# Optimization experiments

Hardware: AMD Instinct MI355X
Metric: run time of the kernel (lower is better)

Reference implementation:

```python
import jax, jax.numpy as jnp
import numpy as np

D_MODEL = 2048
HEADS = 32
HEAD_DIM = 64   # D_MODEL // HEADS
STATE = 256
KCONV = 4
CHUNK = 64
EPS = 1e-5
CONV_DIM = D_MODEL + 2 * STATE          # 2560 (n_groups=1)
PROJ = D_MODEL + CONV_DIM + HEADS       # 4640 (z | xBC | dt)
BATCH, SEQ = 2, 2048


def rmsnorm(x, w, eps=EPS):
    return x * jax.lax.rsqrt(jnp.mean(x * x, axis=-1, keepdims=True) + eps) * w


def setup_inputs() -> dict:
    key = jax.random.key(0)
    ks = jax.random.split(key, 8)
    x = jax.random.normal(ks[0], (BATCH, SEQ, D_MODEL), jnp.float32)
    norm_w = jnp.ones((D_MODEL,), jnp.float32)
    w_in = jax.random.normal(ks[1], (D_MODEL, PROJ), jnp.float32) * 0.02
    conv_w = jax.random.normal(ks[2], (CONV_DIM, KCONV), jnp.float32) * 0.2
    conv_b = jnp.zeros((CONV_DIM,), jnp.float32)
    # HF-style dt init: softplus(dt_bias) uniform-log in [1e-3, 1e-1]
    dt0 = jnp.exp(jax.random.uniform(ks[3], (HEADS,)) * (np.log(0.1) - np.log(0.001)) + np.log(0.001))
    dt_bias = dt0 + jnp.log(-jnp.expm1(-dt0))
    A_log = jnp.log(jnp.arange(1, HEADS + 1, dtype=jnp.float32))
    D_skip = jnp.ones((HEADS,), jnp.float32)
    gnorm_w = jnp.ones((D_MODEL,), jnp.float32)
    w_out = jax.random.normal(ks[4], (D_MODEL, D_MODEL), jnp.float32) * 0.02
    wo_w = jax.random.normal(ks[5], (D_MODEL, D_MODEL), jnp.float32) * 0.02
    return {"x": x, "norm_w": norm_w, "w_in": w_in, "conv_w": conv_w, "conv_b": conv_b,
            "dt_bias": dt_bias, "A_log": A_log, "D_skip": D_skip, "gnorm_w": gnorm_w,
            "w_out": w_out, "wo_w": wo_w}


def reference(x, norm_w, w_in, conv_w, conv_b, dt_bias, A_log, D_skip, gnorm_w, w_out, wo_w):
    b, L, _ = x.shape
    nc = L // CHUNK
    # pre-RMSNorm
    xn = rmsnorm(x, norm_w)
    # in_proj and split: z | xBC | dt
    proj = xn @ w_in
    z = proj[..., :D_MODEL]
    xBC = proj[..., D_MODEL:D_MODEL + CONV_DIM]
    dt = proj[..., D_MODEL + CONV_DIM:]                      # [b,L,H]
    # causal depthwise conv1d (kernel 4) + SiLU
    xp = jnp.pad(xBC, ((0, 0), (KCONV - 1, 0), (0, 0)))
    conv = conv_b + sum(xp[:, k:k + L] * conv_w[:, k] for k in range(KCONV))
    conv = jax.nn.silu(conv)
    xs = conv[..., :D_MODEL].reshape(b, L, HEADS, HEAD_DIM)  # SSM input
    Bm = conv[..., D_MODEL:D_MODEL + STATE]                  # [b,L,N] (n_groups=1)
    Cm = conv[..., D_MODEL + STATE:]                         # [b,L,N]
    dt = jax.nn.softplus(dt + dt_bias)                       # [b,L,H], >0
    A = -jnp.exp(A_log)                                      # [H]
    # ---- Mamba2 chunked selective scan (chunk_size=64) ----
    def ck(a):
        return a.reshape(b, nc, CHUNK, *a.shape[2:])
    xs_c, dt_c, B_c, C_c = ck(xs), ck(dt), ck(Bm), ck(Cm)
    Adt = dt_c * A                                           # [b,c,l,h] (<=0)
    Acs = jnp.cumsum(Adt, axis=2)
    # intra-chunk (diagonal blocks)
    seg = Acs[:, :, :, None, :] - Acs[:, :, None, :, :]      # [b,c,l,s,h]
    idx = jnp.arange(CHUNK)
    mask = (idx[:, None] >= idx[None, :])[None, None, :, :, None]
    Lmat = jnp.where(mask, jnp.exp(seg), 0.0)                # [b,c,l,s,h]
    CB = jnp.einsum('bcln,bcsn->bcls', C_c, B_c)
    xt = xs_c * dt_c[..., None]                              # [b,c,l,h,p]
    Y_diag = jnp.einsum('bclsh,bcshp->bclhp', CB[..., None] * Lmat, xt)
    # chunk-final states
    decay_states = jnp.exp(Acs[:, :, -1:, :] - Acs)          # [b,c,l,h]
    states = jnp.einsum('bcln,bclh,bclhp->bchpn', B_c, decay_states, xt)
    # inter-chunk recurrence (scan over nc chunks only)
    chunk_decay = jnp.exp(Acs[:, :, -1, :])                  # [b,c,h]
    def step(S, inp):
        dec, st = inp
        return S * dec[:, :, None, None] + st, S
    S0 = jnp.zeros((b, HEADS, HEAD_DIM, STATE), x.dtype)
    _, prev = jax.lax.scan(step, S0, (jnp.moveaxis(chunk_decay, 1, 0), jnp.moveaxis(states, 1, 0)))
    prev = jnp.moveaxis(prev, 0, 1)                          # [b,c,h,p,n] state at chunk start
    Y_off = jnp.einsum('bcln,bchpn,bclh->bclhp', C_c, prev, jnp.exp(Acs))
    y = (Y_diag + Y_off).reshape(b, L, HEADS, HEAD_DIM) + D_skip[None, None, :, None] * xs
    y = y.reshape(b, L, D_MODEL)
    # gated RMSNorm, out_proj, then wo
    y = rmsnorm(y * jax.nn.silu(z), gnorm_w)
    return (y @ w_out) @ wo_w
```

## Files before the change

### kernel.cpp

```cpp
#include <hip/hip_runtime.h>
#include <math.h>

#define D_MODEL 2048
#define HEADS 32
#define HEAD_DIM 64
#define STATE 256
#define KCONV 4
#define CHUNK 64
#define NC 32
#define SEQL 2048
#define BATCHN 2
#define CONV_DIMN 2560
#define PROJ_DIM 4640
#define PROJB_W 4608
#define EPSF 1e-5f
#define BL (BATCHN * SEQL)

typedef __attribute__((ext_vector_type(8))) short short8;
typedef __attribute__((ext_vector_type(4))) short short4v;
typedef __attribute__((ext_vector_type(4))) float f32x4;

__device__ __forceinline__ short f2bf(float f) {
  unsigned u = __builtin_bit_cast(unsigned, f);
  u = (u + 0x7fffu + ((u >> 16) & 1u)) >> 16;
  return (short)u;
}
__device__ __forceinline__ float b2f(short s) {
  unsigned u = ((unsigned)(unsigned short)s) << 16;
  return __builtin_bit_cast(float, u);
}
__device__ __forceinline__ void gld16(const void* g, void* l) {
  __builtin_amdgcn_global_load_lds((const __attribute__((address_space(1))) unsigned int*)g,
                                   (__attribute__((address_space(3))) unsigned int*)l,
                                   16, 0, 0);
}

__global__ __launch_bounds__(256) void rmsnorm_bf16_k(const float* __restrict__ x,
                                                      const float* __restrict__ w,
                                                      short* __restrict__ out) {
  int row = blockIdx.x;
  int t = threadIdx.x;
  const float4* x4 = (const float4*)(x + (size_t)row * D_MODEL);
  float4 va = x4[2 * t], vb = x4[2 * t + 1];
  float ss = va.x * va.x + va.y * va.y + va.z * va.z + va.w * va.w +
             vb.x * vb.x + vb.y * vb.y + vb.z * vb.z + vb.w * vb.w;
  #pragma unroll
  for (int off = 32; off > 0; off >>= 1) ss += __shfl_down(ss, off);
  __shared__ float ws_[4];
  if ((t & 63) == 0) ws_[t >> 6] = ss;
  __syncthreads();
  float tot = ws_[0] + ws_[1] + ws_[2] + ws_[3];
  float scale = rsqrtf(tot / (float)D_MODEL + EPSF);
  const float4* w4 = (const float4*)w;
  float4 wa = w4[2 * t], wb = w4[2 * t + 1];
  short tmp[8];
  tmp[0] = f2bf(va.x * scale * wa.x); tmp[1] = f2bf(va.y * scale * wa.y);
  tmp[2] = f2bf(va.z * scale * wa.z); tmp[3] = f2bf(va.w * scale * wa.w);
  tmp[4] = f2bf(vb.x * scale * wb.x); tmp[5] = f2bf(vb.y * scale * wb.y);
  tmp[6] = f2bf(vb.z * scale * wb.z); tmp[7] = f2bf(vb.w * scale * wb.w);
  *(int4*)(out + (size_t)row * D_MODEL + t * 8) = *(int4*)tmp;
}

__global__ __launch_bounds__(256) void transpose_bf16_k(const float* __restrict__ W,
                                                        short* __restrict__ WT,
                                                        int K, int ncols, int stride) {
  __shared__ float tile[32][33];
  int bn = blockIdx.x * 32, bk = blockIdx.y * 32;
  int tx = threadIdx.x & 31, ty = threadIdx.x >> 5;
  #pragma unroll
  for (int i = 0; i < 32; i += 8) {
    int k = bk + ty + i, n = bn + tx;
    tile[ty + i][tx] = (n < ncols) ? W[(size_t)k * stride + n] : 0.f;
  }
  __syncthreads();
  #pragma unroll
  for (int i = 0; i < 32; i += 8) {
    int n = bn + ty + i, k = bk + tx;
    if (n < ncols) WT[(size_t)n * K + k] = f2bf(tile[tx][ty + i]);
  }
}

__global__ __launch_bounds__(256) void dtg_k(const short* __restrict__ xnb,
                                             const short* __restrict__ wdtT,
                                             float* __restrict__ dtraw) {
  __shared__ float red[4][32][32];
  int t = threadIdx.x;
  int lane = t & 63, w = t >> 6;
  int mr = lane & 15, q = lane >> 4;
  int m0 = blockIdx.x * 32;
  f32x4 acc[2][2] = {};
  for (int ks = 0; ks < 16; ks++) {
    int k = w * 512 + ks * 32 + q * 8;
    short8 af[2], bfr[2];
    #pragma unroll
    for (int i = 0; i < 2; i++)
      af[i] = *(const short8*)&xnb[(size_t)(m0 + i * 16 + mr) * D_MODEL + k];
    #pragma unroll
    for (int i = 0; i < 2; i++)
      bfr[i] = *(const short8*)&wdtT[(size_t)(i * 16 + mr) * D_MODEL + k];
    #pragma unroll
    for (int mi = 0; mi < 2; mi++)
      #pragma unroll
      for (int ni = 0; ni < 2; ni++)
        acc[mi][ni] = __builtin_amdgcn_mfma_f32_16x16x32_bf16(af[mi], bfr[ni], acc[mi][ni], 0, 0, 0);
  }
  #pragma unroll
  for (int mi = 0; mi < 2; mi++)
    #pragma unroll
    for (int ni = 0; ni < 2; ni++)
      #pragma unroll
      for (int r = 0; r < 4; r++)
        red[w][mi * 16 + q * 4 + r][ni * 16 + mr] = acc[mi][ni][r];
  __syncthreads();
  #pragma unroll
  for (int i = 0; i < 4; i++) {
    int e = t + 256 * i;
    int row = e >> 5, col = e & 31;
    dtraw[(size_t)(m0 + row) * HEADS + col] =
        red[0][row][col] + red[1][row][col] + red[2][row][col] + red[3][row][col];
  }
}

template<bool BF16OUT>
__global__ __launch_bounds__(512, 4) void gemm128_k(const short* __restrict__ A,
                                                    const short* __restrict__ BT,
                                                    void* __restrict__ Cout,
                                                    int M, int N, int K) {
  constexpr int ABUF = 128 * 32;
  constexpr int BUFS = ABUF + 8192;
  constexpr int LPT = 3;
  __shared__ short lds[3 * BUFS];

  const int t = threadIdx.x;
  const int lane = t & 63, w = t >> 6;
  const int mr = lane & 15, q = lane >> 4;
  const int cq8 = (q ^ ((mr >> 1) & 3)) * 8;
  const int stj = ((lane & 3) ^ ((lane >> 3) & 3)) * 8;
  const int str = lane >> 2;

  const int nbx = N >> 8;
  const int nwg = nbx * (M >> 7);
  const int cpx = nwg >> 3;
  const int bid = blockIdx.x;
  const int swz = (bid & 7) * cpx + (bid >> 3);
  const int bx = swz % nbx, by = swz / nbx;
  const int m0 = by * 128, n0 = bx * 256;

  const int NT = K >> 5;
  f32x4 acc[8][2] = {};

  auto STAGE = [&](int tile, int buf) {
    short* dst = &lds[buf * BUFS];
    const int kb = tile * 32 + stj;
    gld16(A + (size_t)(m0 + w * 16 + str) * K + kb, dst + w * 512);
    const short* gB = BT + (size_t)(n0 + w * 32 + str) * K + kb;
    short* dB = dst + ABUF + w * 1024;
    gld16(gB, dB);
    gld16(gB + (size_t)16 * K, dB + 512);
  };

  STAGE(0, 0); STAGE(1, 1);
  asm volatile("s_waitcnt vmcnt(%0)" :: "n"(LPT) : "memory");
  __builtin_amdgcn_s_barrier();

  int bufc = 0;
  for (int tt = 0; tt < NT; ++tt) {
    const short* sA = &lds[bufc * BUFS];
    const short* sB = sA + ABUF;
    if (tt + 2 < NT) STAGE(tt + 2, bufc >= 1 ? bufc - 1 : 2);
    short8 af[4], bfr[2];
    #pragma unroll
    for (int ni = 0; ni < 2; ni++)
      bfr[ni] = *(const short8*)&sB[(w * 32 + ni * 16 + mr) * 32 + cq8];
    #pragma unroll
    for (int mi = 0; mi < 4; mi++)
      af[mi] = *(const short8*)&sA[(mi * 16 + mr) * 32 + cq8];
    __builtin_amdgcn_s_setprio(1);
    #pragma unroll
    for (int mi = 0; mi < 4; mi++)
      #pragma unroll
      for (int ni = 0; ni < 2; ni++)
        acc[mi][ni] = __builtin_amdgcn_mfma_f32_16x16x32_bf16(af[mi], bfr[ni], acc[mi][ni], 0, 0, 0);
    __builtin_amdgcn_s_setprio(0);
    #pragma unroll
    for (int mi = 0; mi < 4; mi++)
      af[mi] = *(const short8*)&sA[(64 + mi * 16 + mr) * 32 + cq8];
    __builtin_amdgcn_s_setprio(1);
    #pragma unroll
    for (int mi = 0; mi < 4; mi++)
      #pragma unroll
      for (int ni = 0; ni < 2; ni++)
        acc[4 + mi][ni] = __builtin_amdgcn_mfma_f32_16x16x32_bf16(af[mi], bfr[ni], acc[4 + mi][ni], 0, 0, 0);
    __builtin_amdgcn_s_setprio(0);
    __builtin_amdgcn_sched_barrier(0);
    if (tt + 2 < NT) asm volatile("s_waitcnt vmcnt(%0)" :: "n"(LPT) : "memory");
    else             asm volatile("s_waitcnt vmcnt(0)" ::: "memory");
    __builtin_amdgcn_s_barrier();
    bufc = (bufc == 2) ? 0 : bufc + 1;
  }

  #pragma unroll
  for (int mi = 0; mi < 8; mi++)
    #pragma unroll
    for (int ni = 0; ni < 2; ni++) {
      const int gm = m0 + mi * 16 + q * 4;
      const int gn = n0 + w * 32 + ni * 16 + mr;
      #pragma unroll
      for (int r = 0; r < 4; r++) {
        if (BF16OUT) ((short*)Cout)[(size_t)(gm + r) * N + gn] = f2bf(acc[mi][ni][r]);
        else         ((float*)Cout)[(size_t)(gm + r) * N + gn] = acc[mi][ni][r];
      }
    }
}

template<bool BF16OUT>
__global__ __launch_bounds__(256, 3) void gemm_t128_k(const short* __restrict__ A,
                                                      const short* __restrict__ BT,
                                                      void* __restrict__ Cout,
                                                      int M, int N, int K) {
  constexpr int ABUF = 128 * 32;
  constexpr int BUFS = ABUF + 128 * 32;
  constexpr int LPT = 4;
  __shared__ short lds[3 * BUFS];

  const int t = threadIdx.x;
  const int lane = t & 63, w = t >> 6;
  const int mr = lane & 15, q = lane >> 4;
  const int cq8 = (q ^ ((mr >> 1) & 3)) * 8;
  const int stj = ((lane & 3) ^ ((lane >> 3) & 3)) * 8;
  const int str = lane >> 2;

  const int nbx = N >> 7;
  const int nwg = nbx * (M >> 7);
  const int cpx = nwg >> 3;
  const int bid = blockIdx.x;
  const int swz = (bid & 7) * cpx + (bid >> 3);
  const int bx = swz % nbx, by = swz / nbx;
  const int m0 = by * 128, n0 = bx * 128;

  const int NT = K >> 5;
  f32x4 acc[8][2] = {};

  auto STAGE = [&](int tile, int buf) {
    short* dst = &lds[buf * BUFS];
    const int kb = tile * 32 + stj;
    #pragma unroll
    for (int cc = 0; cc < 2; cc++) {
      gld16(A + (size_t)(m0 + w * 32 + cc * 16 + str) * K + kb,
            dst + (w * 32 + cc * 16) * 32);
      gld16(BT + (size_t)(n0 + w * 32 + cc * 16 + str) * K + kb,
            dst + ABUF + (w * 32 + cc * 16) * 32);
    }
  };

  STAGE(0, 0); STAGE(1, 1);
  asm volatile("s_waitcnt vmcnt(%0)" :: "n"(LPT) : "memory");
  __builtin_amdgcn_s_barrier();

  int bufc = 0;
  for (int tt = 0; tt < NT; ++tt) {
    const short* sA = &lds[bufc * BUFS];
    const short* sB = sA + ABUF;
    if (tt + 2 < NT) STAGE(tt + 2, bufc >= 1 ? bufc - 1 : 2);
    short8 af[4], bfr[2];
    #pragma unroll
    for (int ni = 0; ni < 2; ni++)
      bfr[ni] = *(const short8*)&sB[(w * 32 + ni * 16 + mr) * 32 + cq8];
    #pragma unroll
    for (int mi = 0; mi < 4; mi++)
      af[mi] = *(const short8*)&sA[(mi * 16 + mr) * 32 + cq8];
    __builtin_amdgcn_s_setprio(1);
    #pragma unroll
    for (int mi = 0; mi < 4; mi++)
      #pragma unroll
      for (int ni = 0; ni < 2; ni++)
        acc[mi][ni] = __builtin_amdgcn_mfma_f32_16x16x32_bf16(af[mi], bfr[ni], acc[mi][ni], 0, 0, 0);
    __builtin_amdgcn_s_setprio(0);
    #pragma unroll
    for (int mi = 0; mi < 4; mi++)
      af[mi] = *(const short8*)&sA[(64 + mi * 16 + mr) * 32 + cq8];
    __builtin_amdgcn_s_setprio(1);
    #pragma unroll
    for (int mi = 0; mi < 4; mi++)
      #pragma unroll
      for (int ni = 0; ni < 2; ni++)
        acc[4 + mi][ni] = __builtin_amdgcn_mfma_f32_16x16x32_bf16(af[mi], bfr[ni], acc[4 + mi][ni], 0, 0, 0);
    __builtin_amdgcn_s_setprio(0);
    __builtin_amdgcn_sched_barrier(0);
    if (tt + 2 < NT) asm volatile("s_waitcnt vmcnt(%0)" :: "n"(LPT) : "memory");
    else             asm volatile("s_waitcnt vmcnt(0)" ::: "memory");
    __builtin_amdgcn_s_barrier();
    bufc = (bufc == 2) ? 0 : bufc + 1;
  }

  #pragma unroll
  for (int mi = 0; mi < 8; mi++)
    #pragma unroll
    for (int ni = 0; ni < 2; ni++) {
      const int gm = m0 + mi * 16 + q * 4;
      const int gn = n0 + w * 32 + ni * 16 + mr;
      #pragma unroll
      for (int r = 0; r < 4; r++) {
        if (BF16OUT) ((short*)Cout)[(size_t)(gm + r) * N + gn] = f2bf(acc[mi][ni][r]);
        else         ((float*)Cout)[(size_t)(gm + r) * N + gn] = acc[mi][ni][r];
      }
    }
}

__global__ __launch_bounds__(256) void conv_silu_k(const short* __restrict__ projb,
                                                   const float* __restrict__ cw,
                                                   const float* __restrict__ cb,
                                                   short* __restrict__ out) {
  int idx = blockIdx.x * 256 + threadIdx.x;
  int ci = idx % (CONV_DIMN / 8);
  int bt = idx / (CONV_DIMN / 8);
  int t = bt & (SEQL - 1);
  int b = bt >> 11;
  int c = ci * 8;
  float4 w4[8];
  #pragma unroll
  for (int j = 0; j < 8; j++) w4[j] = ((const float4*)cw)[c + j];
  float acc[8];
  {
    float4 b0 = ((const float4*)(cb + c))[0], b1 = ((const float4*)(cb + c))[1];
    acc[0] = b0.x; acc[1] = b0.y; acc[2] = b0.z; acc[3] = b0.w;
    acc[4] = b1.x; acc[5] = b1.y; acc[6] = b1.z; acc[7] = b1.w;
  }
  #pragma unroll
  for (int k = 0; k < KCONV; k++) {
    int tt = t - (KCONV - 1) + k;
    if (tt < 0) continue;
    short8 v = *(const short8*)&projb[((size_t)(b * SEQL + tt)) * PROJB_W + D_MODEL + c];
    #pragma unroll
    for (int j = 0; j < 8; j++) {
      float wv = (k == 0) ? w4[j].x : (k == 1) ? w4[j].y : (k == 2) ? w4[j].z : w4[j].w;
      acc[j] += b2f(v[j]) * wv;
    }
  }
  short o[8];
  #pragma unroll
  for (int j = 0; j < 8; j++) o[j] = f2bf(acc[j] / (1.f + expf(-acc[j])));
  *(int4*)&out[(size_t)bt * CONV_DIMN + c] = *(int4*)o;
}

__global__ __launch_bounds__(256) void dt_acs_k(const float* __restrict__ dtraw,
                                                const float* __restrict__ dt_bias,
                                                const float* __restrict__ A_log,
                                                float* __restrict__ dtb, float* __restrict__ acsb) {
  int bc = blockIdx.x;
  int b = bc / NC, c = bc % NC;
  int t = threadIdx.x;
  int l = t & 63, w = t >> 6;
  size_t base = ((size_t)(b * SEQL + c * CHUNK + l)) * HEADS;
  #pragma unroll
  for (int i = 0; i < 8; i++) {
    int h = w * 8 + i;
    float raw = dtraw[base + h] + dt_bias[h];
    float dt = raw > 20.f ? raw : log1pf(expf(raw));
    float adt = -expf(A_log[h]) * dt;
    float cs = adt;
    #pragma unroll
    for (int off = 1; off < 64; off <<= 1) {
      float v = __shfl_up(cs, off);
      if (l >= off) cs += v;
    }
    dtb[base + h] = dt;
    acsb[base + h] = cs;
  }
}

__global__ __launch_bounds__(256) void cb_k(const short* __restrict__ convb,
                                            short* __restrict__ CB) {
  int bc = blockIdx.x;
  int b = bc / NC, c = bc % NC;
  __shared__ float sC[64][65];
  __shared__ float sB[64][65];
  int t = threadIdx.x;
  int s = t & 63;
  int lb = (t >> 6) * 16;
  float acc[16] = {};
  size_t rowb = ((size_t)(b * SEQL + c * CHUNK)) * CONV_DIMN;
  for (int nt = 0; nt < 4; nt++) {
    __syncthreads();
    #pragma unroll
    for (int i = 0; i < 16; i++) {
      int e = t + 256 * i;
      int r = e >> 6, col = e & 63;
      sC[r][col] = b2f(convb[rowb + (size_t)r * CONV_DIMN + (D_MODEL + STATE) + nt * 64 + col]);
      sB[r][col] = b2f(convb[rowb + (size_t)r * CONV_DIMN + D_MODEL + nt * 64 + col]);
    }
    __syncthreads();
    for (int n = 0; n < 64; n++) {
      float bv = sB[s][n];
      #pragma unroll
      for (int j = 0; j < 16; j++) acc[j] += sC[lb + j][n] * bv;
    }
  }
  size_t ob = ((size_t)bc) * 64 * 64;
  #pragma unroll
  for (int j = 0; j < 16; j++) CB[ob + (size_t)(lb + j) * 64 + s] = f2bf(acc[j]);
}

__global__ __launch_bounds__(256) void chunk_states_k(const short* __restrict__ convb,
                                                      const float* __restrict__ dtb,
                                                      const float* __restrict__ acsb,
                                                      short* __restrict__ G0,
                                                      short* __restrict__ G1) {
  int blk = blockIdx.x & 1023;
  int b = blockIdx.x >> 10;
  short* G = b ? G1 : G0;
  int h = blk & 31, c = blk >> 5;
  __shared__ __align__(16) short sXT[64][72];
  __shared__ __align__(16) short sBT[256][72];
  __shared__ float swt[64];
  int t = threadIdx.x;
  size_t rowb = ((size_t)(b * SEQL + c * CHUNK)) * CONV_DIMN;
  size_t ab = ((size_t)(b * SEQL + c * CHUNK)) * HEADS;
  if (t < 64) {
    float a = acsb[ab + (size_t)t * HEADS + h];
    float alast = acsb[ab + (size_t)63 * HEADS + h];
    swt[t] = expf(alast - a) * dtb[ab + (size_t)t * HEADS + h];
  }
  __syncthreads();
  #pragma unroll
  for (int i = 0; i < 4; i++) {
    int e = t + 256 * i;
    int l = e >> 4, p4 = (e & 15) * 4;
    short4v v = *(const short4v*)&convb[rowb + (size_t)l * CONV_DIMN + h * HEAD_DIM + p4];
    float wt = swt[l];
    short vv[4] = {v.x, v.y, v.z, v.w};
    #pragma unroll
    for (int j = 0; j < 4; j++) {
      int p = p4 + j;
      sXT[p][((((l >> 3) ^ ((p >> 2) & 7)) << 3) | (l & 7))] = f2bf(b2f(vv[j]) * wt);
    }
  }
  #pragma unroll
  for (int i = 0; i < 16; i++) {
    int e = t + 256 * i;
    int l = e >> 6, n4 = (e & 63) * 4;
    short4v v = *(const short4v*)&convb[rowb + (size_t)l * CONV_DIMN + D_MODEL + n4];
    short vv[4] = {v.x, v.y, v.z, v.w};
    #pragma unroll
    for (int j = 0; j < 4; j++) {
      int n = n4 + j;
      sBT[n][((((l >> 3) ^ ((n >> 2) & 7)) << 3) | (l & 7))] = vv[j];
    }
  }
  __syncthreads();
  int lane = t & 63, w = t >> 6;
  int mr = lane & 15, q = lane >> 4;
  f32x4 acc[4][4] = {};
  #pragma unroll
  for (int ks = 0; ks < 2; ks++) {
    short8 af[4], bfr[4];
    #pragma unroll
    for (int mi = 0; mi < 4; mi++) {
      int p = mi * 16 + mr;
      af[mi] = *(const short8*)&sXT[p][(((ks * 4 + q) ^ ((p >> 2) & 7)) << 3)];
    }
    #pragma unroll
    for (int ni = 0; ni < 4; ni++) {
      int n = w * 64 + ni * 16 + mr;
      bfr[ni] = *(const short8*)&sBT[n][(((ks * 4 + q) ^ ((n >> 2) & 7)) << 3)];
    }
    #pragma unroll
    for (int mi = 0; mi < 4; mi++)
      #pragma unroll
      for (int ni = 0; ni < 4; ni++)
        acc[mi][ni] = __builtin_amdgcn_mfma_f32_16x16x32_bf16(af[mi], bfr[ni], acc[mi][ni], 0, 0, 0);
  }
  size_t gb = (size_t)blk * (64 * 256);
  #pragma unroll
  for (int mi = 0; mi < 4; mi++)
    #pragma unroll
    for (int ni = 0; ni < 4; ni++)
      #pragma unroll
      for (int r = 0; r < 4; r++)
        G[gb + (size_t)(mi * 16 + q * 4 + r) * 256 + w * 64 + ni * 16 + mr] = f2bf(acc[mi][ni][r]);
}

__global__ __launch_bounds__(256) void scan_states_k(short* __restrict__ G0,
                                                     short* __restrict__ G1,
                                                     const float* __restrict__ acsb) {
  int gid = blockIdx.x * 256 + threadIdx.x;
  int b = gid >> 16;
  int tid = gid & 65535;
  short* G = b ? G1 : G0;
  int n8 = tid & 31, p = (tid >> 5) & 63, h = tid >> 11;
  float S[8] = {};
  for (int c = 0; c < NC; c++) {
    size_t base = (((size_t)(c * HEADS + h) * 64) + p) * 256 + n8 * 8;
    short gs[8];
    *(int4*)gs = *(const int4*)&G[base];
    short ws8[8];
    #pragma unroll
    for (int j = 0; j < 8; j++) ws8[j] = f2bf(S[j]);
    *(int4*)&G[base] = *(int4*)ws8;
    float dec = expf(acsb[((size_t)(b * SEQL + c * CHUNK + 63)) * HEADS + h]);
    #pragma unroll
    for (int j = 0; j < 8; j++) S[j] = S[j] * dec + b2f(gs[j]);
  }
}

__global__ __launch_bounds__(256) void y_fused_k(const short* __restrict__ convb,
                                                 const short* __restrict__ CBb,
                                                 const short* __restrict__ G0,
                                                 const short* __restrict__ G1,
                                                 const float* __restrict__ dtb,
                                                 const float* __restrict__ acsb,
                                                 const float* __restrict__ D_skip,
                                                 float* __restrict__ Y) {
  int blk = blockIdx.x & 1023;
  int b = blockIdx.x >> 10;
  const short* G = b ? G1 : G0;
  int h = blk & 31, c = blk >> 5;
  __shared__ __align__(16) short sM[64][72];
  __shared__ __align__(16) short sXT[64][72];
  __shared__ float sacs[64], sdt[64], sea[64];
  int t = threadIdx.x;
  int lane = t & 63, w = t >> 6;
  size_t rowb = ((size_t)(b * SEQL + c * CHUNK)) * CONV_DIMN;
  size_t ab = ((size_t)(b * SEQL + c * CHUNK)) * HEADS;
  size_t cbbase = ((size_t)(b * NC + c)) * 64 * 64;
  if (t < 64) {
    float a = acsb[ab + (size_t)t * HEADS + h];
    sacs[t] = a;
    sea[t] = expf(a);
    sdt[t] = dtb[ab + (size_t)t * HEADS + h];
  }
  __syncthreads();
  #pragma unroll
  for (int i = 0; i < 16; i++) {
    int e = t + 256 * i;
    int r = e >> 6, col = e & 63;
    float m = 0.f;
    if (col <= r)
      m = b2f(CBb[cbbase + (size_t)r * 64 + col]) * expf(sacs[r] - sacs[col]) * sdt[col];
    sM[r][col] = f2bf(m);
  }
  #pragma unroll
  for (int i = 0; i < 4; i++) {
    int e = t + 256 * i;
    int l = e >> 4, p4 = (e & 15) * 4;
    short4v v = *(const short4v*)&convb[rowb + (size_t)l * CONV_DIMN + h * HEAD_DIM + p4];
    short vv[4] = {v.x, v.y, v.z, v.w};
    #pragma unroll
    for (int j = 0; j < 4; j++) {
      int p = p4 + j;
      sXT[p][((((l >> 3) ^ ((p >> 2) & 7)) << 3) | (l & 7))] = vv[j];
    }
  }
  __syncthreads();
  int mr = lane & 15, q = lane >> 4;
  int wm = (w & 1) * 32, wn = (w >> 1) * 32;
  f32x4 acc1[2][2] = {}, acc2[2][2] = {};
  #pragma unroll
  for (int ks = 0; ks < 2; ks++) {
    short8 af[2], bfr[2];
    #pragma unroll
    for (int mi = 0; mi < 2; mi++)
      af[mi] = *(const short8*)&sM[wm + mi * 16 + mr][ks * 32 + q * 8];
    #pragma unroll
    for (int ni = 0; ni < 2; ni++) {
      int p = wn + ni * 16 + mr;
      bfr[ni] = *(const short8*)&sXT[p][(((ks * 4 + q) ^ ((p >> 2) & 7)) << 3)];
    }
    #pragma unroll
    for (int mi = 0; mi < 2; mi++)
      #pragma unroll
      for (int ni = 0; ni < 2; ni++)
        acc1[mi][ni] = __builtin_amdgcn_mfma_f32_16x16x32_bf16(af[mi], bfr[ni], acc1[mi][ni], 0, 0, 0);
  }
  const short* Crow = convb + rowb + (D_MODEL + STATE);
  size_t gbase = (size_t)blk * (64 * 256);
  #pragma unroll
  for (int st = 0; st < 8; st++) {
    short8 af[2], bfr[2];
    #pragma unroll
    for (int mi = 0; mi < 2; mi++) {
      int l = wm + mi * 16 + mr;
      af[mi] = *(const short8*)&Crow[(size_t)l * CONV_DIMN + st * 32 + q * 8];
    }
    #pragma unroll
    for (int ni = 0; ni < 2; ni++) {
      int p = wn + ni * 16 + mr;
      bfr[ni] = *(const short8*)&G[gbase + (size_t)p * 256 + st * 32 + q * 8];
    }
    #pragma unroll
    for (int mi = 0; mi < 2; mi++)
      #pragma unroll
      for (int ni = 0; ni < 2; ni++)
        acc2[mi][ni] = __builtin_amdgcn_mfma_f32_16x16x32_bf16(af[mi], bfr[ni], acc2[mi][ni], 0, 0, 0);
  }
  float dsk = D_skip[h];
  size_t ybase = ((size_t)(b * SEQL + c * CHUNK)) * D_MODEL + h * HEAD_DIM;
  #pragma unroll
  for (int mi = 0; mi < 2; mi++)
    #pragma unroll
    for (int ni = 0; ni < 2; ni++) {
      int p = wn + ni * 16 + mr;
      #pragma unroll
      for (int r = 0; r < 4; r++) {
        int l = wm + mi * 16 + q * 4 + r;
        float xsv = b2f(sXT[p][((((l >> 3) ^ ((p >> 2) & 7)) << 3) | (l & 7))]);
        Y[ybase + (size_t)l * D_MODEL + p] =
            acc1[mi][ni][r] + sea[l] * acc2[mi][ni][r] + dsk * xsv;
      }
    }
}

__global__ __launch_bounds__(256) void gated_norm_bf16_k(const float* __restrict__ Y,
                                                         const short* __restrict__ projb,
                                                         const float* __restrict__ gw,
                                                         short* __restrict__ out) {
  int row = blockIdx.x;
  int t = threadIdx.x;
  const float4* y4 = (const float4*)(Y + (size_t)row * D_MODEL);
  float4 ya = y4[2 * t], yb = y4[2 * t + 1];
  short zt[8];
  *(int4*)zt = *(const int4*)(projb + (size_t)row * PROJB_W + t * 8);
  float g[8];
  float yv[8] = {ya.x, ya.y, ya.z, ya.w, yb.x, yb.y, yb.z, yb.w};
  float ss = 0.f;
  #pragma unroll
  for (int i = 0; i < 8; i++) {
    float z = b2f(zt[i]);
    g[i] = yv[i] * (z / (1.f + expf(-z)));
    ss += g[i] * g[i];
  }
  #pragma unroll
  for (int off = 32; off > 0; off >>= 1) ss += __shfl_down(ss, off);
  __shared__ float ws_[4];
  if ((t & 63) == 0) ws_[t >> 6] = ss;
  __syncthreads();
  float tot = ws_[0] + ws_[1] + ws_[2] + ws_[3];
  float scale = rsqrtf(tot / (float)D_MODEL + EPSF);
  const float4* g4 = (const float4*)gw;
  float4 wa = g4[2 * t], wb = g4[2 * t + 1];
  float wv[8] = {wa.x, wa.y, wa.z, wa.w, wb.x, wb.y, wb.z, wb.w};
  short tmp[8];
  #pragma unroll
  for (int i = 0; i < 8; i++) tmp[i] = f2bf(g[i] * scale * wv[i]);
  *(int4*)(out + (size_t)row * D_MODEL + t * 8) = *(int4*)tmp;
}

extern "C" void kernel_launch(void* const* d_in, const int* in_sizes, int n_in,
                              void* d_out, int out_size, void* d_ws, size_t ws_size,
                              hipStream_t stream) {
  const float* x       = (const float*)d_in[0];
  const float* norm_w  = (const float*)d_in[1];
  const float* w_in    = (const float*)d_in[2];
  const float* conv_w  = (const float*)d_in[3];
  const float* conv_b  = (const float*)d_in[4];
  const float* dt_bias = (const float*)d_in[5];
  const float* A_log   = (const float*)d_in[6];
  const float* D_skip  = (const float*)d_in[7];
  const float* gnorm_w = (const float*)d_in[8];
  const float* w_out   = (const float*)d_in[9];
  const float* wo_w    = (const float*)d_in[10];
  float* out = (float*)d_out;

  float* ws    = (float*)d_ws;
  short* xnb   = (short*)ws;
  short* w_inT = (short*)(ws + 4194304);
  short* projb = (short*)(ws + 8912896);
  short* convb = (short*)(ws + 18350080);
  float* dtraw = ws + 23592960;
  float* dtb   = ws + 23724032;
  float* acsb  = ws + 23855104;
  short* CBb   = (short*)(ws + 23986176);
  float* Yb    = ws + 24117248;
  short* w_outT= (short*)(ws + 32505856);
  short* wo_wT = (short*)(ws + 34603008);
  short* wdtT  = (short*)dtb;
  short* G0    = (short*)ws;
  short* G1    = (short*)out;
  short* Yg    = convb;
  short* t1b   = (short*)ws;

  rmsnorm_bf16_k<<<BL, 256, 0, stream>>>(x, norm_w, xnb);
  transpose_bf16_k<<<dim3(PROJB_W / 32, D_MODEL / 32), 256, 0, stream>>>(w_in, w_inT, D_MODEL, PROJB_W, PROJ_DIM);
  transpose_bf16_k<<<dim3(1, D_MODEL / 32), 256, 0, stream>>>(w_in + D_MODEL + CONV_DIMN, wdtT, D_MODEL, HEADS, PROJ_DIM);
  transpose_bf16_k<<<dim3(D_MODEL / 32, D_MODEL / 32), 256, 0, stream>>>(w_out, w_outT, D_MODEL, D_MODEL, D_MODEL);
  transpose_bf16_k<<<dim3(D_MODEL / 32, D_MODEL / 32), 256, 0, stream>>>(wo_w, wo_wT, D_MODEL, D_MODEL, D_MODEL);
  dtg_k<<<BL / 32, 256, 0, stream>>>(xnb, wdtT, dtraw);
  gemm128_k<true><<<(BL / 128) * (PROJB_W / 256), 512, 0, stream>>>(xnb, w_inT, projb, BL, PROJB_W, D_MODEL);
  conv_silu_k<<<(BL * (CONV_DIMN / 8)) / 256, 256, 0, stream>>>(projb, conv_w, conv_b, convb);
  dt_acs_k<<<BATCHN * NC, 256, 0, stream>>>(dtraw, dt_bias, A_log, dtb, acsb);
  cb_k<<<BATCHN * NC, 256, 0, stream>>>(convb, CBb);
  chunk_states_k<<<BATCHN * NC * HEADS, 256, 0, stream>>>(convb, dtb, acsb, G0, G1);
  scan_states_k<<<512, 256, 0, stream>>>(G0, G1, acsb);
  y_fused_k<<<BATCHN * NC * HEADS, 256, 0, stream>>>(convb, CBb, G0, G1, dtb, acsb, D_skip, Yb);
  gated_norm_bf16_k<<<BL, 256, 0, stream>>>(Yb, projb, gnorm_w, Yg);
  gemm_t128_k<true><<<(BL / 128) * (D_MODEL / 128), 256, 0, stream>>>(Yg, w_outT, t1b, BL, D_MODEL, D_MODEL);
  gemm_t128_k<false><<<(BL / 128) * (D_MODEL / 128), 256, 0, stream>>>(t1b, wo_wT, out, BL, D_MODEL, D_MODEL);
}
```

Baseline: 570.8 us.

## Use 8-wave 128x128 GEMM for output projections and merge CB/dt kernels

After: 563.4 us. About the same (-1.3%).

```diff
diff --git a/kernel.cpp b/kernel.cpp
--- a/kernel.cpp
+++ b/kernel.cpp
@@ -214,13 +214,13 @@
 }
 
 template<bool BF16OUT>
-__global__ __launch_bounds__(256, 3) void gemm_t128_k(const short* __restrict__ A,
+__global__ __launch_bounds__(512, 4) void gemm_s128_k(const short* __restrict__ A,
                                                       const short* __restrict__ BT,
                                                       void* __restrict__ Cout,
                                                       int M, int N, int K) {
   constexpr int ABUF = 128 * 32;
   constexpr int BUFS = ABUF + 128 * 32;
-  constexpr int LPT = 4;
+  constexpr int LPT = 2;
   __shared__ short lds[3 * BUFS];
 
   const int t = threadIdx.x;
@@ -229,6 +229,7 @@
   const int cq8 = (q ^ ((mr >> 1) & 3)) * 8;
   const int stj = ((lane & 3) ^ ((lane >> 3) & 3)) * 8;
   const int str = lane >> 2;
+  const int wm = w & 1, wn = w >> 1;
 
   const int nbx = N >> 7;
   const int nwg = nbx * (M >> 7);
@@ -239,18 +240,13 @@
   const int m0 = by * 128, n0 = bx * 128;
 
   const int NT = K >> 5;
-  f32x4 acc[8][2] = {};
+  f32x4 acc[4][2] = {};
 
   auto STAGE = [&](int tile, int buf) {
     short* dst = &lds[buf * BUFS];
     const int kb = tile * 32 + stj;
-    #pragma unroll
-    for (int cc = 0; cc < 2; cc++) {
-      gld16(A + (size_t)(m0 + w * 32 + cc * 16 + str) * K + kb,
-            dst + (w * 32 + cc * 16) * 32);
-      gld16(BT + (size_t)(n0 + w * 32 + cc * 16 + str) * K + kb,
-            dst + ABUF + (w * 32 + cc * 16) * 32);
-    }
+    gld16(A + (size_t)(m0 + w * 16 + str) * K + kb, dst + w * 512);
+    gld16(BT + (size_t)(n0 + w * 16 + str) * K + kb, dst + ABUF + w * 512);
   };
 
   STAGE(0, 0); STAGE(1, 1);
@@ -265,26 +261,16 @@
     short8 af[4], bfr[2];
     #pragma unroll
     for (int ni = 0; ni < 2; ni++)
-      bfr[ni] = *(const short8*)&sB[(w * 32 + ni * 16 + mr) * 32 + cq8];
+      bfr[ni] = *(const short8*)&sB[(wn * 32 + ni * 16 + mr) * 32 + cq8];
     #pragma unroll
     for (int mi = 0; mi < 4; mi++)
-      af[mi] = *(const short8*)&sA[(mi * 16 + mr) * 32 + cq8];
+      af[mi] = *(const short8*)&sA[(wm * 64 + mi * 16 + mr) * 32 + cq8];
     __builtin_amdgcn_s_setprio(1);
     #pragma unroll
     for (int mi = 0; mi < 4; mi++)
       #pragma unroll
       for (int ni = 0; ni < 2; ni++)
         acc[mi][ni] = __builtin_amdgcn_mfma_f32_16x16x32_bf16(af[mi], bfr[ni], acc[mi][ni], 0, 0, 0);
-    __builtin_amdgcn_s_setprio(0);
-    #pragma unroll
-    for (int mi = 0; mi < 4; mi++)
-      af[mi] = *(const short8*)&sA[(64 + mi * 16 + mr) * 32 + cq8];
-    __builtin_amdgcn_s_setprio(1);
-    #pragma unroll
-    for (int mi = 0; mi < 4; mi++)
-      #pragma unroll
-      for (int ni = 0; ni < 2; ni++)
-        acc[4 + mi][ni] = __builtin_amdgcn_mfma_f32_16x16x32_bf16(af[mi], bfr[ni], acc[4 + mi][ni], 0, 0, 0);
     __builtin_amdgcn_s_setprio(0);
     __builtin_amdgcn_sched_barrier(0);
     if (tt + 2 < NT) asm volatile("s_waitcnt vmcnt(%0)" :: "n"(LPT) : "memory");
@@ -294,11 +280,11 @@
   }
 
   #pragma unroll
-  for (int mi = 0; mi < 8; mi++)
+  for (int mi = 0; mi < 4; mi++)
     #pragma unroll
     for (int ni = 0; ni < 2; ni++) {
-      const int gm = m0 + mi * 16 + q * 4;
-      const int gn = n0 + w * 32 + ni * 16 + mr;
+      const int gm = m0 + wm * 64 + mi * 16 + q * 4;
+      const int gn = n0 + wn * 32 + ni * 16 + mr;
       #pragma unroll
       for (int r = 0; r < 4; r++) {
         if (BF16OUT) ((short*)Cout)[(size_t)(gm + r) * N + gn] = f2bf(acc[mi][ni][r]);
@@ -343,62 +329,64 @@
   *(int4*)&out[(size_t)bt * CONV_DIMN + c] = *(int4*)o;
 }
 
-__global__ __launch_bounds__(256) void dt_acs_k(const float* __restrict__ dtraw,
-                                                const float* __restrict__ dt_bias,
-                                                const float* __restrict__ A_log,
-                                                float* __restrict__ dtb, float* __restrict__ acsb) {
-  int bc = blockIdx.x;
-  int b = bc / NC, c = bc % NC;
-  int t = threadIdx.x;
-  int l = t & 63, w = t >> 6;
-  size_t base = ((size_t)(b * SEQL + c * CHUNK + l)) * HEADS;
-  #pragma unroll
-  for (int i = 0; i < 8; i++) {
-    int h = w * 8 + i;
-    float raw = dtraw[base + h] + dt_bias[h];
-    float dt = raw > 20.f ? raw : log1pf(expf(raw));
-    float adt = -expf(A_log[h]) * dt;
-    float cs = adt;
-    #pragma unroll
-    for (int off = 1; off < 64; off <<= 1) {
-      float v = __shfl_up(cs, off);
-      if (l >= off) cs += v;
-    }
-    dtb[base + h] = dt;
-    acsb[base + h] = cs;
-  }
-}
-
-__global__ __launch_bounds__(256) void cb_k(const short* __restrict__ convb,
-                                            short* __restrict__ CB) {
-  int bc = blockIdx.x;
-  int b = bc / NC, c = bc % NC;
-  __shared__ float sC[64][65];
-  __shared__ float sB[64][65];
-  int t = threadIdx.x;
-  int s = t & 63;
-  int lb = (t >> 6) * 16;
-  float acc[16] = {};
-  size_t rowb = ((size_t)(b * SEQL + c * CHUNK)) * CONV_DIMN;
-  for (int nt = 0; nt < 4; nt++) {
-    __syncthreads();
-    #pragma unroll
-    for (int i = 0; i < 16; i++) {
-      int e = t + 256 * i;
-      int r = e >> 6, col = e & 63;
-      sC[r][col] = b2f(convb[rowb + (size_t)r * CONV_DIMN + (D_MODEL + STATE) + nt * 64 + col]);
-      sB[r][col] = b2f(convb[rowb + (size_t)r * CONV_DIMN + D_MODEL + nt * 64 + col]);
-    }
-    __syncthreads();
-    for (int n = 0; n < 64; n++) {
-      float bv = sB[s][n];
-      #pragma unroll
-      for (int j = 0; j < 16; j++) acc[j] += sC[lb + j][n] * bv;
-    }
-  }
-  size_t ob = ((size_t)bc) * 64 * 64;
-  #pragma unroll
-  for (int j = 0; j < 16; j++) CB[ob + (size_t)(lb + j) * 64 + s] = f2bf(acc[j]);
+__global__ __launch_bounds__(256) void cbdt_k(const short* __restrict__ convb,
+                                              short* __restrict__ CB,
+                                              const float* __restrict__ dtraw,
+                                              const float* __restrict__ dt_bias,
+                                              const float* __restrict__ A_log,
+                                              float* __restrict__ dtb,
+                                              float* __restrict__ acsb) {
+  if (blockIdx.x < BATCHN * NC) {
+    int bc = blockIdx.x;
+    int b = bc / NC, c = bc % NC;
+    __shared__ float sC[64][65];
+    __shared__ float sB[64][65];
+    int t = threadIdx.x;
+    int s = t & 63;
+    int lb = (t >> 6) * 16;
+    float acc[16] = {};
+    size_t rowb = ((size_t)(b * SEQL + c * CHUNK)) * CONV_DIMN;
+    for (int nt = 0; nt < 4; nt++) {
+      __syncthreads();
+      #pragma unroll
+      for (int i = 0; i < 16; i++) {
+        int e = t + 256 * i;
+        int r = e >> 6, col = e & 63;
+        sC[r][col] = b2f(convb[rowb + (size_t)r * CONV_DIMN + (D_MODEL + STATE) + nt * 64 + col]);
+        sB[r][col] = b2f(convb[rowb + (size_t)r * CONV_DIMN + D_MODEL + nt * 64 + col]);
+      }
+      __syncthreads();
+      for (int n = 0; n < 64; n++) {
+        float bv = sB[s][n];
+        #pragma unroll
+        for (int j = 0; j < 16; j++) acc[j] += sC[lb + j][n] * bv;
+      }
+    }
+    size_t ob = ((size_t)bc) * 64 * 64;
+    #pragma unroll
+    for (int j = 0; j < 16; j++) CB[ob + (size_t)(lb + j) * 64 + s] = f2bf(acc[j]);
+  } else {
+    int bc = blockIdx.x - BATCHN * NC;
+    int b = bc / NC, c = bc % NC;
+    int t = threadIdx.x;
+    int l = t & 63, w = t >> 6;
+    size_t base = ((size_t)(b * SEQL + c * CHUNK + l)) * HEADS;
+    #pragma unroll
+    for (int i = 0; i < 8; i++) {
+      int h = w * 8 + i;
+      float raw = dtraw[base + h] + dt_bias[h];
+      float dt = raw > 20.f ? raw : log1pf(expf(raw));
+      float adt = -expf(A_log[h]) * dt;
+      float cs = adt;
+      #pragma unroll
+      for (int off = 1; off < 64; off <<= 1) {
+        float v = __shfl_up(cs, off);
+        if (l >= off) cs += v;
+      }
+      dtb[base + h] = dt;
+      acsb[base + h] = cs;
+    }
+  }
 }
 
 __global__ __launch_bounds__(256) void chunk_states_k(const short* __restrict__ convb,
@@ -687,12 +675,11 @@
   dtg_k<<<BL / 32, 256, 0, stream>>>(xnb, wdtT, dtraw);
   gemm128_k<true><<<(BL / 128) * (PROJB_W / 256), 512, 0, stream>>>(xnb, w_inT, projb, BL, PROJB_W, D_MODEL);
   conv_silu_k<<<(BL * (CONV_DIMN / 8)) / 256, 256, 0, stream>>>(projb, conv_w, conv_b, convb);
-  dt_acs_k<<<BATCHN * NC, 256, 0, stream>>>(dtraw, dt_bias, A_log, dtb, acsb);
-  cb_k<<<BATCHN * NC, 256, 0, stream>>>(convb, CBb);
+  cbdt_k<<<2 * BATCHN * NC, 256, 0, stream>>>(convb, CBb, dtraw, dt_bias, A_log, dtb, acsb);
   chunk_states_k<<<BATCHN * NC * HEADS, 256, 0, stream>>>(convb, dtb, acsb, G0, G1);
   scan_states_k<<<512, 256, 0, stream>>>(G0, G1, acsb);
   y_fused_k<<<BATCHN * NC * HEADS, 256, 0, stream>>>(convb, CBb, G0, G1, dtb, acsb, D_skip, Yb);
   gated_norm_bf16_k<<<BL, 256, 0, stream>>>(Yb, projb, gnorm_w, Yg);
-  gemm_t128_k<true><<<(BL / 128) * (D_MODEL / 128), 256, 0, stream>>>(Yg, w_outT, t1b, BL, D_MODEL, D_MODEL);
-  gemm_t128_k<false><<<(BL / 128) * (D_MODEL / 128), 256, 0, stream>>>(t1b, wo_wT, out, BL, D_MODEL, D_MODEL);
-}
+  gemm_s128_k<true><<<(BL / 128) * (D_MODEL / 128), 512, 0, stream>>>(Yg, w_outT, t1b, BL, D_MODEL, D_MODEL);
+  gemm_s128_k<false><<<(BL / 128) * (D_MODEL / 128), 512, 0, stream>>>(t1b, wo_wT, out, BL, D_MODEL, D_MODEL);
+}
```
